# Optimization experiments

Measured on AMD Instinct MI355X. Metric: run time of the kernel, lower is better.

## Reference

```python
import jax, jax.numpy as jnp
import numpy as np

# SSFM configuration (matches init_kwargs; amplification/noise disabled)
ALPHA = 0.046       # attenuation [1/km]
BETA2 = -21.67      # GVD [ps^2/km]
GAMMA = 1.27        # nonlinearity [1/km/W]
LENGTH = 80.0       # fiber length [km]
N_SSFM = 64         # number of SSFM steps
HALF_WIN = 100      # half Hamming window length
DT = 1.0            # normalized sample duration


def _make_window(n):
    # tf.signal.hamming_window(2*HALF_WIN) is periodic: 0.54 - 0.46*cos(2*pi*k/L)
    L = 2 * HALF_WIN
    w = (0.54 - 0.46 * jnp.cos(2.0 * np.float32(np.pi) * jnp.arange(L, dtype=jnp.float32) / np.float32(L)))
    win = jnp.concatenate([w[:HALF_WIN], jnp.ones((n - L,), jnp.float32), w[HALF_WIN:]])
    return win.astype(jnp.complex64)


def _freq_vector(n):
    # sionna.utils.time_frequency_vector: f = (arange(n) - n/2) / (n * dt)
    return ((jnp.arange(n, dtype=jnp.float32) - np.float32(n / 2)) / np.float32(n * DT))


def setup_inputs() -> dict:
    key = jax.random.key(0)
    k1, k2 = jax.random.split(key)
    shape = (4, 262144)
    x_real = 0.05 * jax.random.normal(k1, shape, dtype=jnp.float32)
    x_imag = 0.05 * jax.random.normal(k2, shape, dtype=jnp.float32)
    return {"x_real": x_real, "x_imag": x_imag}


def reference(x_real, x_imag):
    x = (x_real + 1j * x_imag).astype(jnp.complex64)  # [B, N]
    n = x.shape[-1]
    f = _freq_vector(n)                                # [N]
    win = _make_window(n)                              # [N] complex
    dz = np.float32(LENGTH / N_SSFM)

    def apply_linear(q, dz_):
        # dispersion: exp(-j * beta2/2 * dz * (2*pi*f)^2), fftshifted
        phase = -(np.float32(BETA2) / 2.0) * dz_ * (2.0 * np.float32(np.pi) * f) ** 2
        disp = jnp.fft.fftshift(jnp.exp(1j * phase).astype(jnp.complex64))
        q = jnp.fft.ifft(jnp.fft.fft(q, axis=-1) * disp, axis=-1)
        # attenuation
        q = q * jnp.exp(np.float32(-ALPHA / 2.0) * dz_).astype(jnp.complex64)
        return q

    def apply_nonlinear(q, dz_):
        phi = (jnp.abs(q) ** 2) * np.float32(GAMMA) * (-dz_)
        return q * jnp.exp(1j * phi)

    # symmetrized SSFM: D(dz/2) [W N(dz) D(dz)]^{n-1} W N(dz) D(dz/2)
    q = apply_linear(x, dz / 2.0)

    def step(q, _):
        q = q * win
        q = apply_nonlinear(q, dz)
        q = apply_linear(q, dz)
        return q, None

    q, _ = jax.lax.scan(step, q, None, length=N_SSFM - 1)

    q = q * win
    q = apply_nonlinear(q, dz)
    q = apply_linear(q, dz / 2.0)

    # return real/imag stacked so the output is a real tensor: [2, B, N]
    return jnp.stack([jnp.real(q), jnp.imag(q)], axis=0)
```

## Files before the change

kernel.cpp:

```cpp
#include <hip/hip_runtime.h>


static constexpr double PI_D = 3.14159265358979323846;

__device__ __forceinline__ float2 cadd(float2 a, float2 b){ return make_float2(a.x+b.x, a.y+b.y); }
__device__ __forceinline__ float2 csub(float2 a, float2 b){ return make_float2(a.x-b.x, a.y-b.y); }
__device__ __forceinline__ float2 cmul(float2 a, float2 b){
  return make_float2(fmaf(a.x, b.x, -(a.y*b.y)), fmaf(a.x, b.y, a.y*b.x));
}

__device__ __forceinline__ int sg(int e){
  int d2 = (e>>6)&7, d1 = (e>>3)&7;
  return e ^ (d2<<3) ^ d1 ^ d2;
}

template<int INV>
__device__ __forceinline__ void dft8(float2 r[8]){
  const float RS = 0.7071067811865476f;
  float2 t0=cadd(r[0],r[4]), t4=csub(r[0],r[4]);
  float2 t1=cadd(r[1],r[5]), t5=csub(r[1],r[5]);
  float2 t2=cadd(r[2],r[6]), t6=csub(r[2],r[6]);
  float2 t3=cadd(r[3],r[7]), t7=csub(r[3],r[7]);
  float2 u1,u2,u3;
  if(!INV){
    u1 = make_float2((t5.x+t5.y)*RS, (t5.y-t5.x)*RS);
    u2 = make_float2(t6.y, -t6.x);
    u3 = make_float2((t7.y-t7.x)*RS, -(t7.x+t7.y)*RS);
  } else {
    u1 = make_float2((t5.x-t5.y)*RS, (t5.x+t5.y)*RS);
    u2 = make_float2(-t6.y, t6.x);
    u3 = make_float2(-(t7.x+t7.y)*RS, (t7.x-t7.y)*RS);
  }
  float2 e0=cadd(t0,t2), e1=csub(t0,t2), e2=cadd(t1,t3), e3=csub(t1,t3);
  float2 f3 = (!INV)? make_float2(e3.y,-e3.x) : make_float2(-e3.y,e3.x);
  r[0]=cadd(e0,e2); r[4]=csub(e0,e2); r[2]=cadd(e1,f3); r[6]=csub(e1,f3);
  float2 o0=cadd(t4,u2), o1=csub(t4,u2), o2=cadd(u1,u3), o3=csub(u1,u3);
  float2 g3 = (!INV)? make_float2(o3.y,-o3.x) : make_float2(-o3.y,o3.x);
  r[1]=cadd(o0,o2); r[5]=csub(o0,o2); r[3]=cadd(o1,g3); r[7]=csub(o1,g3);
}

template<int INV>
__device__ __forceinline__ void fft512(float2 r[8], int l, float2* ex){
  const float W512 = (float)(2.0*PI_D/512.0);
  const float W64  = (float)(2.0*PI_D/64.0);
  int j = l>>3, p = l&7;
  float s,c;
  if(!INV){
    dft8<0>(r);
    __sincosf(-W512*(float)l, &s, &c);
    float2 w = make_float2(c,s), cur = w;
    #pragma unroll
    for(int q=1;q<8;q++){ r[q]=cmul(r[q],cur); cur=cmul(cur,w); }
    #pragma unroll
    for(int q=0;q<8;q++) ex[sg(l + 64*q)] = r[q];
    #pragma unroll
    for(int m=0;m<8;m++) r[m] = ex[sg(64*j + p + 8*m)];
    dft8<0>(r);
    __sincosf(-W64*(float)p, &s, &c);
    w = make_float2(c,s); cur = w;
    #pragma unroll
    for(int q=1;q<8;q++){ r[q]=cmul(r[q],cur); cur=cmul(cur,w); }
    #pragma unroll
    for(int q=0;q<8;q++) ex[sg(64*j + p + 8*q)] = r[q];
    #pragma unroll
    for(int m=0;m<8;m++) r[m] = ex[sg(64*j + 8*p + m)];
    dft8<0>(r);
  } else {
    dft8<1>(r);
    #pragma unroll
    for(int m=0;m<8;m++) ex[sg(64*j + 8*p + m)] = r[m];
    #pragma unroll
    for(int q=0;q<8;q++) r[q] = ex[sg(64*j + p + 8*q)];
    __sincosf(W64*(float)p, &s, &c);
    float2 w = make_float2(c,s), cur = w;
    #pragma unroll
    for(int q=1;q<8;q++){ r[q]=cmul(r[q],cur); cur=cmul(cur,w); }
    dft8<1>(r);
    #pragma unroll
    for(int m=0;m<8;m++) ex[sg(64*j + p + 8*m)] = r[m];
    #pragma unroll
    for(int q=0;q<8;q++) r[q] = ex[sg(l + 64*q)];
    __sincosf(W512*(float)l, &s, &c);
    w = make_float2(c,s); cur = w;
    #pragma unroll
    for(int q=1;q<8;q++){ r[q]=cmul(r[q],cur); cur=cmul(cur,w); }
    dft8<1>(r);
  }
}

__global__ __launch_bounds__(512) void kSetup(float2* __restrict__ dispF, float2* __restrict__ dispH){
  int m  = blockIdx.x*512 + threadIdx.x;
  int k1 = m >> 9, k2 = m & 511;
  int k  = k1 + (k2 << 9);
  int ks = (k < 131072) ? k : k - 262144;
  float fv  = (float)ks / 262144.0f;
  float tpf = 6.28318548202514648f * fv;
  float e2  = tpf * tpf;
  const float bh = 10.8350000381469727f;
  float phF = (bh * 1.25f)  * e2;
  float phH = (bh * 0.625f) * e2;
  double sF,cF,sH,cH;
  sincos((double)phF, &sF, &cF);
  sincos((double)phH, &sH, &cH);
  const float aco = -0.023000000044703484f;
  double scF = exp((double)(aco*1.25f))  / 262144.0;
  double scH = exp((double)(aco*0.625f)) / 262144.0;
  dispF[m] = make_float2((float)(cF*scF), (float)(sF*scF));
  dispH[m] = make_float2((float)(cH*scH), (float)(sH*scH));
}

__global__ __launch_bounds__(512) void kA(const float2* __restrict__ src, float2* __restrict__ dst,
                                          const float2* __restrict__ disp){
  __shared__ float2 ex[8][512];
  int t = threadIdx.x, w = t>>6, l = t&63;
  int k1 = blockIdx.x*8 + w;
  size_t base = ((size_t)blockIdx.y<<18) + (size_t)k1*512;
  const float2* s = src + base;
  float2* d = dst + base;
  float2 r[8];
  #pragma unroll
  for(int m=0;m<8;m++) r[m] = s[l + 64*m];
  fft512<0>(r, l, ex[w]);
  int p=l&7, j=l>>3;
  const float2* dp = disp + (size_t)k1*512;
  #pragma unroll
  for(int q=0;q<8;q++) r[q] = cmul(r[q], dp[64*q + 8*p + j]);
  fft512<1>(r, l, ex[w]);
  float c1 = (float)(2.0*PI_D/262144.0)*(float)k1;
  float sb,cb,ss,cs;
  __sincosf(c1*(float)l, &sb, &cb);
  __sincosf(c1*64.0f,    &ss, &cs);
  float2 tw = make_float2(cb,sb), st = make_float2(cs,ss);
  #pragma unroll
  for(int m=0;m<8;m++){ d[l+64*m] = cmul(r[m], tw); tw = cmul(tw, st); }
}

template<int MODE>
__global__ __launch_bounds__(512) void kB(const float* __restrict__ xr, const float* __restrict__ xi,
                                          const float2* __restrict__ src, float2* __restrict__ dst,
                                          float* __restrict__ outp){
  __shared__ float2 tile[8][514];
  int t=threadIdx.x, w=t>>6, l=t&63;
  int c0 = blockIdx.x*8;
  size_t base = ((size_t)blockIdx.y<<18);
  #pragma unroll
  for(int i=0;i<8;i++){
    int rr = i*64 + (t>>3), cc = t&7;
    size_t a = base + (size_t)rr*512 + (size_t)(c0 + cc);
    if(MODE==0) tile[cc][sg(rr)] = make_float2(xr[a], xi[a]);
    else        tile[cc][sg(rr)] = src[a];
  }
  __syncthreads();
  float2 r[8];
  int p=l&7, j=l>>3;
  int n2 = c0 + w;
  if(MODE==0){
    #pragma unroll
    for(int m=0;m<8;m++) r[m] = tile[w][sg(l + 64*m)];
  } else {
    #pragma unroll
    for(int q=0;q<8;q++) r[q] = tile[w][sg(64*q + 8*p + j)];
    fft512<1>(r, l, tile[w]);
  }
  if(MODE==1){
    #pragma unroll
    for(int m=0;m<8;m++){
      int n1 = l + 64*m;
      float wv = 1.0f;
      if(n1==0 && n2<100){
        float ang = (6.28318548202514648f*(float)n2)*0.005f;
        wv = 0.54f - 0.46f*cosf(ang);
      } else if(n1==511 && n2>=412){
        float ang = (6.28318548202514648f*(float)(n2-312))*0.005f;
        wv = 0.54f - 0.46f*cosf(ang);
      }
      float2 qv = make_float2(r[m].x*wv, r[m].y*wv);
      float aq2 = fmaf(qv.x,qv.x, qv.y*qv.y);
      float phi = (aq2 * 1.26999998092651367f) * (-1.25f);
      float sp,cp; __sincosf(phi,&sp,&cp);
      r[m] = cmul(qv, make_float2(cp,sp));
    }
  }
  if(MODE==2){
    #pragma unroll
    for(int m=0;m<8;m++) tile[w][sg(l + 64*m)] = r[m];
    __syncthreads();
    #pragma unroll
    for(int i=0;i<8;i++){
      int rr = i*64 + (t>>3), cc = t&7;
      float2 v = tile[cc][sg(rr)];
      size_t a = base + (size_t)rr*512 + (size_t)(c0 + cc);
      outp[a] = v.x;
      outp[(size_t)(1<<20) + a] = v.y;
    }
    return;
  }
  fft512<0>(r, l, tile[w]);
  float c1 = -(float)(2.0*PI_D/262144.0)*(float)n2;
  float sb,cb,ss,cs;
  __sincosf(c1*(float)(8*p + j), &sb, &cb);
  __sincosf(c1*64.0f,            &ss, &cs);
  float2 tw=make_float2(cb,sb), st=make_float2(cs,ss);
  #pragma unroll
  for(int q=0;q<8;q++){ r[q]=cmul(r[q],tw); tw=cmul(tw,st); }
  #pragma unroll
  for(int q=0;q<8;q++) tile[w][sg(64*q + 8*p + j)] = r[q];
  __syncthreads();
  #pragma unroll
  for(int i=0;i<8;i++){
    int rr = i*64 + (t>>3), cc = t&7;
    dst[base + (size_t)rr*512 + (size_t)(c0 + cc)] = tile[cc][sg(rr)];
  }
}

extern "C" void kernel_launch(void* const* d_in, const int* in_sizes, int n_in,
                              void* d_out, int out_size, void* d_ws, size_t ws_size,
                              hipStream_t stream) {
  (void)in_sizes; (void)n_in; (void)out_size; (void)ws_size;
  const float* xr = (const float*)d_in[0];
  const float* xi = (const float*)d_in[1];
  float* out = (float*)d_out;
  char* ws = (char*)d_ws;
  float2* buf1  = (float2*)ws;
  float2* buf2  = (float2*)(ws + ((size_t)8<<20));
  float2* dispF = (float2*)(ws + ((size_t)16<<20));
  float2* dispH = (float2*)(ws + ((size_t)18<<20));

  dim3 blk(512), g(64,4);
  kSetup<<<dim3(512), blk, 0, stream>>>(dispF, dispH);

  kB<0><<<g, blk, 0, stream>>>(xr, xi, nullptr, buf1, nullptr);
  kA<<<g, blk, 0, stream>>>(buf1, buf2, dispH);
  for(int i=0;i<63;i++){
    kB<1><<<g, blk, 0, stream>>>(nullptr, nullptr, buf2, buf1, nullptr);
    kA<<<g, blk, 0, stream>>>(buf1, buf2, dispF);
  }
  kB<1><<<g, blk, 0, stream>>>(nullptr, nullptr, buf2, buf1, nullptr);
  kA<<<g, blk, 0, stream>>>(buf1, buf2, dispH);
  kB<2><<<g, blk, 0, stream>>>(nullptr, nullptr, buf2, nullptr, out);
}
```

Measured before the change: 1.394 ms.

## Fuse all SSFM steps into one persistent cooperative kernel with grid barriers

Replaces the roughly 130 separate kernel launches with a single cooperative persistent kernel of 256 blocks. The blocks step through all FFT passes and separate them with a software grid barrier built on global atomics. Twiddle factors, dispersion coefficients and window weights are computed once into registers per thread instead of being recomputed or reloaded every pass. This removes launch gaps and repeated sincos work, at the cost of higher register pressure (launch bounds 512,2), a spin-wait barrier, and a fallback to the old path if the cooperative launch fails.

```diff
diff --git a/kernel.cpp b/kernel.cpp
--- a/kernel.cpp
+++ b/kernel.cpp
@@ -7,6 +7,9 @@
 __device__ __forceinline__ float2 csub(float2 a, float2 b){ return make_float2(a.x-b.x, a.y-b.y); }
 __device__ __forceinline__ float2 cmul(float2 a, float2 b){
   return make_float2(fmaf(a.x, b.x, -(a.y*b.y)), fmaf(a.x, b.y, a.y*b.x));
+}
+__device__ __forceinline__ float2 cmulc(float2 a, float2 b){
+  return make_float2(fmaf(a.x, b.x, a.y*b.y), fmaf(a.y, b.x, -(a.x*b.y)));
 }
 
 __device__ __forceinline__ int sg(int e){
@@ -39,6 +42,43 @@
   r[1]=cadd(o0,o2); r[5]=csub(o0,o2); r[3]=cadd(o1,g3); r[7]=csub(o1,g3);
 }
 
+__device__ __forceinline__ void fwd512(float2 r[8], int l, int p, int j,
+                                       const float2* t1, const float2* t2, float2* ex){
+  dft8<0>(r);
+  #pragma unroll
+  for(int q=1;q<8;q++) r[q]=cmul(r[q],t1[q-1]);
+  #pragma unroll
+  for(int q=0;q<8;q++) ex[sg(l+64*q)] = r[q];
+  #pragma unroll
+  for(int m=0;m<8;m++) r[m] = ex[sg(64*j+p+8*m)];
+  dft8<0>(r);
+  #pragma unroll
+  for(int q=1;q<8;q++) r[q]=cmul(r[q],t2[q-1]);
+  #pragma unroll
+  for(int q=0;q<8;q++) ex[sg(64*j+p+8*q)] = r[q];
+  #pragma unroll
+  for(int m=0;m<8;m++) r[m] = ex[sg(64*j+8*p+m)];
+  dft8<0>(r);
+}
+__device__ __forceinline__ void inv512(float2 r[8], int l, int p, int j,
+                                       const float2* t1, const float2* t2, float2* ex){
+  dft8<1>(r);
+  #pragma unroll
+  for(int m=0;m<8;m++) ex[sg(64*j+8*p+m)] = r[m];
+  #pragma unroll
+  for(int q=0;q<8;q++) r[q] = ex[sg(64*j+p+8*q)];
+  #pragma unroll
+  for(int q=1;q<8;q++) r[q]=cmulc(r[q],t2[q-1]);
+  dft8<1>(r);
+  #pragma unroll
+  for(int m=0;m<8;m++) ex[sg(64*j+p+8*m)] = r[m];
+  #pragma unroll
+  for(int q=0;q<8;q++) r[q] = ex[sg(l+64*q)];
+  #pragma unroll
+  for(int q=1;q<8;q++) r[q]=cmulc(r[q],t1[q-1]);
+  dft8<1>(r);
+}
+
 template<int INV>
 __device__ __forceinline__ void fft512(float2 r[8], int l, float2* ex){
   const float W512 = (float)(2.0*PI_D/512.0);
@@ -88,7 +128,9 @@
   }
 }
 
-__global__ __launch_bounds__(512) void kSetup(float2* __restrict__ dispF, float2* __restrict__ dispH){
+__global__ __launch_bounds__(512) void kSetup(float2* __restrict__ dispF, float2* __restrict__ dispH,
+                                              int* __restrict__ bar){
+  if (blockIdx.x==0 && threadIdx.x<128) bar[threadIdx.x]=0;
   int m  = blockIdx.x*512 + threadIdx.x;
   int k1 = m >> 9, k2 = m & 511;
   int k  = k1 + (k2 << 9);
@@ -213,6 +255,181 @@
   }
 }
 
+__device__ __forceinline__ void gsync(int* bar){
+  __syncthreads();
+  if (threadIdx.x == 0){
+    __threadfence();
+    int* cnt = bar;
+    int* gen = bar + 64;
+    int g = __hip_atomic_load(gen, __ATOMIC_RELAXED, __HIP_MEMORY_SCOPE_AGENT);
+    if (__hip_atomic_fetch_add(cnt, 1, __ATOMIC_ACQ_REL, __HIP_MEMORY_SCOPE_AGENT)
+        == (int)gridDim.x - 1){
+      __hip_atomic_store(cnt, 0, __ATOMIC_RELAXED, __HIP_MEMORY_SCOPE_AGENT);
+      __hip_atomic_store(gen, g + 1, __ATOMIC_RELEASE, __HIP_MEMORY_SCOPE_AGENT);
+    } else {
+      while (__hip_atomic_load(gen, __ATOMIC_RELAXED, __HIP_MEMORY_SCOPE_AGENT) == g)
+        __builtin_amdgcn_s_sleep(1);
+    }
+    __threadfence();
+  }
+  __syncthreads();
+}
+
+__global__ __launch_bounds__(512, 2) void ssfm_all(
+    const float* __restrict__ xr, const float* __restrict__ xi,
+    float* __restrict__ outp,
+    float2* __restrict__ buf1, float2* __restrict__ buf2,
+    const float2* __restrict__ dispF, const float2* __restrict__ dispH,
+    int* __restrict__ bar)
+{
+  __shared__ float2 tile[8][514];
+  const int t=threadIdx.x, w=t>>6, l=t&63, p=l&7, j=l>>3;
+  const int bi=blockIdx.x;
+  const int lb=((bi&7)<<5)|(bi>>3);
+  const int b=lb>>6, g=lb&63;
+  const size_t base=(size_t)b<<18;
+  const int k1=g*8+w, c0=g*8, n2=c0+w;
+  float2* exch = tile[w];
+
+  float2 t1[7], t2[7], twA[8], twB[8], dpF[8], dpH[8];
+  #pragma unroll
+  for(int q=1;q<8;q++){
+    double s,c;
+    sincos(-2.0*PI_D*(double)(l*q)/512.0,&s,&c); t1[q-1]=make_float2((float)c,(float)s);
+    sincos(-2.0*PI_D*(double)(p*q)/64.0,&s,&c);  t2[q-1]=make_float2((float)c,(float)s);
+  }
+  #pragma unroll
+  for(int m=0;m<8;m++){
+    double s,c;
+    sincos(2.0*PI_D*(double)(k1*(l+64*m))/262144.0,&s,&c);
+    twA[m]=make_float2((float)c,(float)s);
+  }
+  #pragma unroll
+  for(int q=0;q<8;q++){
+    double s,c;
+    sincos(-2.0*PI_D*(double)(n2*(64*q+8*p+j))/262144.0,&s,&c);
+    twB[q]=make_float2((float)c,(float)s);
+    int di=k1*512+64*q+8*p+j;
+    dpF[q]=dispF[di]; dpH[q]=dispH[di];
+  }
+  float wvH=1.0f, wvT=1.0f;
+  if(l==0  && n2<100)  wvH=0.54f-0.46f*cosf((6.28318548202514648f*(float)n2)*0.005f);
+  if(l==63 && n2>=412) wvT=0.54f-0.46f*cosf((6.28318548202514648f*(float)(n2-312))*0.005f);
+
+  {
+    #pragma unroll
+    for(int i=0;i<8;i++){
+      int rr=i*64+(t>>3), cc=t&7;
+      size_t a=base+(size_t)rr*512+(size_t)(c0+cc);
+      tile[cc][sg(rr)]=make_float2(xr[a], xi[a]);
+    }
+    __syncthreads();
+    float2 r[8];
+    #pragma unroll
+    for(int m=0;m<8;m++) r[m]=exch[sg(l+64*m)];
+    fwd512(r,l,p,j,t1,t2,exch);
+    #pragma unroll
+    for(int q=0;q<8;q++) r[q]=cmul(r[q],twB[q]);
+    #pragma unroll
+    for(int q=0;q<8;q++) exch[sg(64*q+8*p+j)]=r[q];
+    __syncthreads();
+    #pragma unroll
+    for(int i=0;i<8;i++){
+      int rr=i*64+(t>>3), cc=t&7;
+      buf1[base+(size_t)rr*512+(size_t)(c0+cc)]=tile[cc][sg(rr)];
+    }
+  }
+  gsync(bar);
+  {
+    const size_t rowbase=base+(size_t)k1*512;
+    float2 r[8];
+    #pragma unroll
+    for(int m=0;m<8;m++) r[m]=buf1[rowbase+l+64*m];
+    fwd512(r,l,p,j,t1,t2,exch);
+    #pragma unroll
+    for(int q=0;q<8;q++) r[q]=cmul(r[q],dpH[q]);
+    inv512(r,l,p,j,t1,t2,exch);
+    #pragma unroll
+    for(int m=0;m<8;m++) buf2[rowbase+l+64*m]=cmul(r[m],twA[m]);
+  }
+  gsync(bar);
+
+  #pragma unroll 1
+  for(int it=0; it<64; ++it){
+    {
+      #pragma unroll
+      for(int i=0;i<8;i++){
+        int rr=i*64+(t>>3), cc=t&7;
+        tile[cc][sg(rr)]=buf2[base+(size_t)rr*512+(size_t)(c0+cc)];
+      }
+      __syncthreads();
+      float2 r[8];
+      #pragma unroll
+      for(int q=0;q<8;q++) r[q]=exch[sg(64*q+8*p+j)];
+      inv512(r,l,p,j,t1,t2,exch);
+      #pragma unroll
+      for(int m=0;m<8;m++){
+        float wv = (m==0)? wvH : ((m==7)? wvT : 1.0f);
+        float2 qv=make_float2(r[m].x*wv, r[m].y*wv);
+        float aq2=fmaf(qv.x,qv.x, qv.y*qv.y);
+        float phi=(aq2*1.26999998092651367f)*(-1.25f);
+        float sp,cp; __sincosf(phi,&sp,&cp);
+        r[m]=cmul(qv,make_float2(cp,sp));
+      }
+      fwd512(r,l,p,j,t1,t2,exch);
+      #pragma unroll
+      for(int q=0;q<8;q++) r[q]=cmul(r[q],twB[q]);
+      #pragma unroll
+      for(int q=0;q<8;q++) exch[sg(64*q+8*p+j)]=r[q];
+      __syncthreads();
+      #pragma unroll
+      for(int i=0;i<8;i++){
+        int rr=i*64+(t>>3), cc=t&7;
+        buf1[base+(size_t)rr*512+(size_t)(c0+cc)]=tile[cc][sg(rr)];
+      }
+    }
+    gsync(bar);
+    {
+      const size_t rowbase=base+(size_t)k1*512;
+      float2 r[8];
+      #pragma unroll
+      for(int m=0;m<8;m++) r[m]=buf1[rowbase+l+64*m];
+      fwd512(r,l,p,j,t1,t2,exch);
+      const bool lastH=(it==63);
+      #pragma unroll
+      for(int q=0;q<8;q++){ float2 dq = lastH? dpH[q] : dpF[q]; r[q]=cmul(r[q],dq); }
+      inv512(r,l,p,j,t1,t2,exch);
+      #pragma unroll
+      for(int m=0;m<8;m++) buf2[rowbase+l+64*m]=cmul(r[m],twA[m]);
+    }
+    gsync(bar);
+  }
+
+  {
+    #pragma unroll
+    for(int i=0;i<8;i++){
+      int rr=i*64+(t>>3), cc=t&7;
+      tile[cc][sg(rr)]=buf2[base+(size_t)rr*512+(size_t)(c0+cc)];
+    }
+    __syncthreads();
+    float2 r[8];
+    #pragma unroll
+    for(int q=0;q<8;q++) r[q]=exch[sg(64*q+8*p+j)];
+    inv512(r,l,p,j,t1,t2,exch);
+    #pragma unroll
+    for(int m=0;m<8;m++) exch[sg(l+64*m)]=r[m];
+    __syncthreads();
+    #pragma unroll
+    for(int i=0;i<8;i++){
+      int rr=i*64+(t>>3), cc=t&7;
+      float2 v=tile[cc][sg(rr)];
+      size_t a=base+(size_t)rr*512+(size_t)(c0+cc);
+      outp[a]=v.x;
+      outp[(size_t)(1<<20)+a]=v.y;
+    }
+  }
+}
+
 extern "C" void kernel_launch(void* const* d_in, const int* in_sizes, int n_in,
                               void* d_out, int out_size, void* d_ws, size_t ws_size,
                               hipStream_t stream) {
@@ -225,17 +442,24 @@
   float2* buf2  = (float2*)(ws + ((size_t)8<<20));
   float2* dispF = (float2*)(ws + ((size_t)16<<20));
   float2* dispH = (float2*)(ws + ((size_t)18<<20));
-
-  dim3 blk(512), g(64,4);
-  kSetup<<<dim3(512), blk, 0, stream>>>(dispF, dispH);
-
-  kB<0><<<g, blk, 0, stream>>>(xr, xi, nullptr, buf1, nullptr);
-  kA<<<g, blk, 0, stream>>>(buf1, buf2, dispH);
-  for(int i=0;i<63;i++){
-    kB<1><<<g, blk, 0, stream>>>(nullptr, nullptr, buf2, buf1, nullptr);
-    kA<<<g, blk, 0, stream>>>(buf1, buf2, dispF);
-  }
-  kB<1><<<g, blk, 0, stream>>>(nullptr, nullptr, buf2, buf1, nullptr);
-  kA<<<g, blk, 0, stream>>>(buf1, buf2, dispH);
-  kB<2><<<g, blk, 0, stream>>>(nullptr, nullptr, buf2, nullptr, out);
-}
+  int*    bar   = (int*)   (ws + ((size_t)20<<20));
+
+  kSetup<<<dim3(512), dim3(512), 0, stream>>>(dispF, dispH, bar);
+
+  void* args[] = {(void*)&xr,(void*)&xi,(void*)&out,(void*)&buf1,(void*)&buf2,
+                  (void*)&dispF,(void*)&dispH,(void*)&bar};
+  hipError_t e = hipLaunchCooperativeKernel((void*)ssfm_all, dim3(256), dim3(512),
+                                            args, 0, stream);
+  if (e != hipSuccess){
+    dim3 blk(512), gdim(64,4);
+    kB<0><<<gdim, blk, 0, stream>>>(xr, xi, nullptr, buf1, nullptr);
+    kA<<<gdim, blk, 0, stream>>>(buf1, buf2, dispH);
+    for(int i=0;i<63;i++){
+      kB<1><<<gdim, blk, 0, stream>>>(nullptr, nullptr, buf2, buf1, nullptr);
+      kA<<<gdim, blk, 0, stream>>>(buf1, buf2, dispF);
+    }
+    kB<1><<<gdim, blk, 0, stream>>>(nullptr, nullptr, buf2, buf1, nullptr);
+    kA<<<gdim, blk, 0, stream>>>(buf1, buf2, dispH);
+    kB<2><<<gdim, blk, 0, stream>>>(nullptr, nullptr, buf2, nullptr, out);
+  }
+}
```

New measurement: 3.611 ms. 159% more time.
